# Optimization experiments

Measured on AMD Instinct MI355X. Metric: run time of the kernel, lower is better.

Reference implementation:

```python
import jax, jax.numpy as jnp
import numpy as np

B, S, D, H, E, F = 2, 1024, 1024, 16, 8, 4096
HD = D // H
EPS = 1e-5


def setup_inputs() -> dict:
    key = jax.random.key(0)
    ks = jax.random.split(key, 16)
    sc = 0.02
    return {
        "src": jax.random.normal(ks[0], (B, S, D), jnp.float32),
        "in_proj_w": jax.random.normal(ks[1], (3 * D, D), jnp.float32) * sc,
        "in_proj_b": jnp.zeros((3 * D,), jnp.float32),
        "out_w": jax.random.normal(ks[2], (D, D), jnp.float32) * sc,
        "out_b": jnp.zeros((D,), jnp.float32),
        "gate_w": jax.random.normal(ks[3], (E, D), jnp.float32) * sc,
        "gate_b": jnp.zeros((E,), jnp.float32),
        "w1": jax.random.normal(ks[4], (E, F, D), jnp.float32) * sc,
        "b1": jnp.zeros((E, F), jnp.float32),
        "w2": jax.random.normal(ks[5], (E, D, F), jnp.float32) * sc,
        "b2": jnp.zeros((E, D), jnp.float32),
        "ln1_g": jnp.ones((D,), jnp.float32),
        "ln1_b": jnp.zeros((D,), jnp.float32),
        "ln2_g": jnp.ones((D,), jnp.float32),
        "ln2_b": jnp.zeros((D,), jnp.float32),
    }


def layer_norm(x, g, b):
    mu = jnp.mean(x, axis=-1, keepdims=True)
    var = jnp.mean(jnp.square(x - mu), axis=-1, keepdims=True)
    return (x - mu) * jax.lax.rsqrt(var + EPS) * g + b


def mha(x, in_proj_w, in_proj_b, out_w, out_b):
    # torch nn.MultiheadAttention, batch_first, self-attention, eval mode
    qkv = x @ in_proj_w.T + in_proj_b  # (B,S,3D)
    q, k, v = jnp.split(qkv, 3, axis=-1)
    q = q.reshape(B, S, H, HD).transpose(0, 2, 1, 3)  # bhsd
    k = k.reshape(B, S, H, HD).transpose(0, 2, 1, 3)
    v = v.reshape(B, S, H, HD).transpose(0, 2, 1, 3)
    scores = jnp.einsum("bhqd,bhkd->bhqk", q, k) / np.sqrt(HD).astype(np.float32)
    attn = jax.nn.softmax(scores, axis=-1)
    o = jnp.einsum("bhqk,bhkd->bhqd", attn, v)
    o = o.transpose(0, 2, 1, 3).reshape(B, S, D)
    return o @ out_w.T + out_b


def moe(x, gate_w, gate_b, w1, b1, w2, b2, top_k=2):
    gate_logits = x @ gate_w.T + gate_b  # (B,S,E)
    topk_logits, topk_idx = jax.lax.top_k(gate_logits, top_k)
    topk_probs = jax.nn.softmax(topk_logits, axis=-1)  # (B,S,K)
    # dense per-expert weight: prob if in top-k else 0
    onehot = jax.nn.one_hot(topk_idx, E, dtype=x.dtype)  # (B,S,K,E)
    w_dense = jnp.einsum("bske,bsk->bse", onehot, topk_probs)
    # faithful to original: all experts computed densely, then mask-weighted
    h = jnp.einsum("bsd,efd->besf", x, w1) + b1[None, :, None, :]
    h = jax.nn.gelu(h, approximate=False)
    eo = jnp.einsum("besf,edf->besd", h, w2) + b2[None, :, None, :]
    out = jnp.einsum("besd,bse->bsd", eo, w_dense)
    usage = jnp.mean(jax.nn.softmax(gate_logits, axis=-1), axis=(0, 1))
    aux_loss = E * jnp.sum(usage ** 2)
    return out, aux_loss


def reference(src, in_proj_w, in_proj_b, out_w, out_b, gate_w, gate_b,
              w1, b1, w2, b2, ln1_g, ln1_b, ln2_g, ln2_b):
    attn_out = mha(src, in_proj_w, in_proj_b, out_w, out_b)
    x = layer_norm(src + attn_out, ln1_g, ln1_b)
    moe_out, aux_loss = moe(x, gate_w, gate_b, w1, b1, w2, b2)
    x = layer_norm(x + moe_out, ln2_g, ln2_b)
    return x, aux_loss
```

## Files before the change

### kernel.cpp

```cpp
#include <hip/hip_runtime.h>
#include <stdint.h>
#include <stddef.h>

#define T_TOK 2048
#define DMODEL 1024
#define NHEAD 16
#define HDIM 64
#define NEXP 8
#define FDIM 4096
#define SLEN 1024
#define NBATCH 2
#define LN_EPS 1e-5f

typedef unsigned short u16;
typedef __attribute__((ext_vector_type(8))) short s16x8;
typedef __attribute__((ext_vector_type(4))) float f32x4;
typedef __attribute__((ext_vector_type(4))) unsigned short u16x4;
typedef __attribute__((ext_vector_type(8))) unsigned short u16x8;

typedef __attribute__((address_space(1))) void gvoid;
typedef __attribute__((address_space(3))) void lvoid;

__device__ __forceinline__ u16 f2bf(float x) {
  union { float f; unsigned int u; } v; v.f = x;
  unsigned int r = v.u + 0x7fffu + ((v.u >> 16) & 1u);
  return (u16)(r >> 16);
}

__device__ __forceinline__ void gl_lds16(const u16* g, u16* lds_base) {
  __builtin_amdgcn_global_load_lds((gvoid*)g, (lvoid*)lds_base, 16, 0, 0);
}

__device__ __forceinline__ void cvt_body(const float* __restrict__ x,
                                         u16* __restrict__ y, long n4) {
  long i = (long)blockIdx.x * 256 + threadIdx.x;
  if (i >= n4) return;
  float4 v = ((const float4*)x)[i];
  u16x4 o;
  o[0] = f2bf(v.x); o[1] = f2bf(v.y); o[2] = f2bf(v.z); o[3] = f2bf(v.w);
  ((u16x4*)y)[i] = o;
}
__global__ __launch_bounds__(256) void cvt_small(const float* x, u16* y, long n4) { cvt_body(x, y, n4); }
__global__ __launch_bounds__(256) void cvt_w1(const float* x, u16* y, long n4) { cvt_body(x, y, n4); }
__global__ __launch_bounds__(256) void cvt_w2(const float* x, u16* y, long n4) { cvt_body(x, y, n4); }

template<int BM, int OUTBF, int DOGELU>
__device__ __forceinline__ void gemm_body(
    const u16* __restrict__ A, long lda,
    const u16* __restrict__ Bp, long ldb,
    char* __restrict__ C, long ldc,
    const float* __restrict__ bias,
    int Mloc, int k0start, int Kc, int m0, int n0) {
  constexpr int AS_BYTES = 2 * BM * 64 * 2;
  constexpr int SMEM_BYTES = AS_BYTES + 2 * 128 * 64 * 2;
  __shared__ __align__(16) char smem[SMEM_BYTES];
  u16 (*As)[BM][64]  = reinterpret_cast<u16(*)[BM][64]>(smem);
  u16 (*Bs)[128][64] = reinterpret_cast<u16(*)[128][64]>(smem + AS_BYTES);

  constexpr int SM = BM / 32;
  constexpr int LPI = BM / 32 + 4;

  int tid = threadIdx.x;
  int lane = tid & 63, w = tid >> 6;
  int lrow = lane >> 3;
  int sg8 = ((lane & 7) ^ lrow) * 8;
  int q = lane >> 4, rr = lane & 15;
  int wm = (w & 1) * (BM / 2), wn = (w >> 1) * 64;
  int NIT = Kc >> 6;

  auto issue = [&](int kt, int b) {
    int k0 = k0start + (kt << 6);
    for (int p = 0; p < BM / 32; p++) {
      int rb = p * 32 + w * 8;
      int gr = m0 + rb + lrow; if (gr > Mloc - 1) gr = Mloc - 1;
      gl_lds16(A + (long)gr * lda + k0 + sg8, &As[b][rb][0]);
    }
    for (int p = 0; p < 4; p++) {
      int rb = p * 32 + w * 8;
      gl_lds16(Bp + (long)(n0 + rb + lrow) * ldb + k0 + sg8, &Bs[b][rb][0]);
    }
  };

  f32x4 acc[SM][4];
  for (int i = 0; i < SM; i++)
    for (int j = 0; j < 4; j++)
      for (int r = 0; r < 4; r++) acc[i][j][r] = 0.f;

  issue(0, 0);
  if (NIT > 1) issue(1, 1);

  int slot0 = ((q ^ (rr & 7)) * 8);
  int slot1 = (((4 + q) ^ (rr & 7)) * 8);

  for (int kt = 0; kt < NIT; kt++) {
    int b = kt & 1;
    if (kt + 1 < NIT)
      asm volatile("s_waitcnt vmcnt(%0)" :: "i"(LPI) : "memory");
    else
      asm volatile("s_waitcnt vmcnt(0)" ::: "memory");
    asm volatile("s_barrier" ::: "memory");

    s16x8 a0[SM], a1[SM], b0[4], b1[4];
    for (int i = 0; i < SM; i++) {
      a0[i] = *(const s16x8*)&As[b][wm + i * 16 + rr][slot0];
      a1[i] = *(const s16x8*)&As[b][wm + i * 16 + rr][slot1];
    }
    for (int j = 0; j < 4; j++) {
      b0[j] = *(const s16x8*)&Bs[b][wn + j * 16 + rr][slot0];
      b1[j] = *(const s16x8*)&Bs[b][wn + j * 16 + rr][slot1];
    }
    asm volatile("s_waitcnt lgkmcnt(0)" ::: "memory");
    asm volatile("s_barrier" ::: "memory");
    if (kt + 2 < NIT) issue(kt + 2, b);

    for (int i = 0; i < SM; i++)
      for (int j = 0; j < 4; j++) {
        acc[i][j] = __builtin_amdgcn_mfma_f32_16x16x32_bf16(a0[i], b0[j], acc[i][j], 0, 0, 0);
        acc[i][j] = __builtin_amdgcn_mfma_f32_16x16x32_bf16(a1[i], b1[j], acc[i][j], 0, 0, 0);
      }
  }

  u16*   Cu = (u16*)smem;
  float* Cf = (float*)smem;
  for (int i = 0; i < SM; i++)
    for (int j = 0; j < 4; j++) {
      int col = wn + j * 16 + rr;
      float bv = bias ? bias[n0 + col] : 0.f;
      for (int r = 0; r < 4; r++) {
        int row = wm + i * 16 + q * 4 + r;
        float v = acc[i][j][r] + bv;
        if (DOGELU) v = 0.5f * v * (1.f + erff(v * 0.70710678118f));
        if (OUTBF) Cu[row * 128 + col] = f2bf(v);
        else       Cf[row * 128 + col] = v;
      }
    }
  __syncthreads();
  if (OUTBF) {
    for (int p = 0; p < BM / 16; p++) {
      int row = p * 16 + (tid >> 4);
      int co  = (tid & 15) * 8;
      if (m0 + row < Mloc) {
        u16x8 vv = *(const u16x8*)&Cu[row * 128 + co];
        *(u16x8*)((u16*)C + (long)(m0 + row) * ldc + n0 + co) = vv;
      }
    }
  } else {
    for (int p = 0; p < BM / 8; p++) {
      int row = p * 8 + (tid >> 5);
      int co  = (tid & 31) * 4;
      if (m0 + row < Mloc) {
        float4 vv = *(const float4*)&Cf[row * 128 + co];
        *(float4*)((float*)C + (long)(m0 + row) * ldc + n0 + co) = vv;
      }
    }
  }
}

__global__ __launch_bounds__(256) void k_qkv(const u16* __restrict__ A,
                                             const u16* __restrict__ B,
                                             u16* __restrict__ C,
                                             const float* __restrict__ bias) {
  gemm_body<64, 1, 0>(A, DMODEL, B, DMODEL, (char*)C, 3 * DMODEL, bias,
                      T_TOK, 0, DMODEL, blockIdx.y * 64, blockIdx.x * 128);
}

__global__ __launch_bounds__(256) void k_outp(const u16* __restrict__ A,
                                              const u16* __restrict__ B,
                                              float* __restrict__ Cpart) {
  int z = blockIdx.z;
  char* C = (char*)(Cpart + (long)z * T_TOK * DMODEL);
  gemm_body<64, 0, 0>(A, DMODEL, B, DMODEL, C, DMODEL, nullptr,
                      T_TOK, z * 512, 512, blockIdx.y * 64, blockIdx.x * 128);
}

__global__ __launch_bounds__(256) void k_ffn1(const u16* __restrict__ Ag,
                                              const u16* __restrict__ Bg,
                                              u16* __restrict__ Cg,
                                              const float* __restrict__ biasg,
                                              const int* __restrict__ cntp,
                                              const int* __restrict__ offp) {
  int z = blockIdx.z;
  int Mloc = cntp[z];
  int m0 = blockIdx.y * 128;
  if (m0 >= Mloc) return;
  long o = offp[z];
  gemm_body<128, 1, 1>(Ag + o * DMODEL, DMODEL,
                       Bg + (long)z * FDIM * DMODEL, DMODEL,
                       (char*)(Cg + o * FDIM), FDIM,
                       biasg + (long)z * FDIM,
                       Mloc, 0, DMODEL, m0, blockIdx.x * 128);
}

__global__ __launch_bounds__(256) void k_ffn2(const u16* __restrict__ Ag,
                                              const u16* __restrict__ Bg,
                                              float* __restrict__ Cg,
                                              const float* __restrict__ biasg,
                                              const int* __restrict__ cntp,
                                              const int* __restrict__ offp) {
  int z = blockIdx.z;
  int Mloc = cntp[z];
  int m0 = blockIdx.y * 64;
  if (m0 >= Mloc) return;
  long o = offp[z];
  gemm_body<64, 0, 0>(Ag + o * FDIM, FDIM,
                      Bg + (long)z * DMODEL * FDIM, FDIM,
                      (char*)(Cg + o * DMODEL), DMODEL,
                      biasg + (long)z * DMODEL,
                      Mloc, 0, FDIM, m0, blockIdx.x * 128);
}

__global__ __launch_bounds__(256) void transpose_v(const u16* __restrict__ qkv,
                                                   u16* __restrict__ vt) {
  __shared__ u16 tile[64][65];
  int s0 = blockIdx.x * 64, bh = blockIdx.y;
  int b = bh >> 4, h = bh & 15;
  int r = threadIdx.x >> 3, c = (threadIdx.x & 7) * 8;
  for (int p = 0; p < 64; p += 32) {
    u16x8 v = *(const u16x8*)&qkv[(long)(b * SLEN + s0 + p + r) * 3072 + 2048 + h * 64 + c];
    for (int j = 0; j < 8; j++) tile[p + r][c + j] = v[j];
  }
  __syncthreads();
  for (int p = 0; p < 64; p += 32) {
    int d = p + r;
    u16x8 v;
    for (int j = 0; j < 8; j++) v[j] = tile[c + j][d];
    *(u16x8*)&vt[((long)bh * 64 + d) * SLEN + s0 + c] = v;
  }
}

__global__ __launch_bounds__(256) void fused_attn(const u16* __restrict__ qkv,
                                                  const u16* __restrict__ vt,
                                                  u16* __restrict__ o2) {
  __shared__ u16 Qs[128][64];
  __shared__ u16 Ks[64][64];
  __shared__ u16 Vs[64][64];
  __shared__ u16 Ps[128][72];

  int qt = blockIdx.x, bh = blockIdx.y;
  int b = bh >> 4, h = bh & 15;
  const u16* base = qkv + (long)b * SLEN * 3072 + h * 64;
  const u16* vbase = vt + (long)bh * HDIM * SLEN;

  int tid = threadIdx.x, lane = tid & 63, w = tid >> 6;
  int lrow = lane >> 3;
  int sg8 = ((lane & 7) ^ lrow) * 8;
  int q = lane >> 4, rr = lane & 15;
  int wm = w * 32;

  for (int p = 0; p < 4; p++) {
    int rb = p * 32 + w * 8;
    gl_lds16(base + (long)(qt * 128 + rb + lrow) * 3072 + sg8, &Qs[rb][0]);
  }

  f32x4 O[2][4];
  float mi[2][4], li[2][4];
  for (int i = 0; i < 2; i++)
    for (int r = 0; r < 4; r++) { mi[i][r] = -1e30f; li[i][r] = 0.f; }
  for (int i = 0; i < 2; i++)
    for (int jn = 0; jn < 4; jn++)
      for (int r = 0; r < 4; r++) O[i][jn][r] = 0.f;

  for (int kt = 0; kt < 16; kt++) {
    __syncthreads();
    for (int p = 0; p < 2; p++) {
      int rb = p * 32 + w * 8;
      gl_lds16(base + (long)(kt * 64 + rb + lrow) * 3072 + 1024 + sg8, &Ks[rb][0]);
      gl_lds16(vbase + (long)(rb + lrow) * SLEN + kt * 64 + sg8, &Vs[rb][0]);
    }
    __syncthreads();

    f32x4 S[2][4];
    for (int i = 0; i < 2; i++)
      for (int j = 0; j < 4; j++)
        for (int r = 0; r < 4; r++) S[i][j][r] = 0.f;
    for (int ks = 0; ks < 2; ks++) {
      int slot = (((ks * 4 + q) ^ (rr & 7)) * 8);
      s16x8 aq0 = *(const s16x8*)&Qs[wm + rr][slot];
      s16x8 aq1 = *(const s16x8*)&Qs[wm + 16 + rr][slot];
      for (int j = 0; j < 4; j++) {
        s16x8 bk = *(const s16x8*)&Ks[j * 16 + rr][slot];
        S[0][j] = __builtin_amdgcn_mfma_f32_16x16x32_bf16(aq0, bk, S[0][j], 0, 0, 0);
        S[1][j] = __builtin_amdgcn_mfma_f32_16x16x32_bf16(aq1, bk, S[1][j], 0, 0, 0);
      }
    }

    for (int i = 0; i < 2; i++) {
      for (int r = 0; r < 4; r++) {
        float mx = -1e30f;
        for (int j = 0; j < 4; j++) mx = fmaxf(mx, S[i][j][r]);
        for (int o = 1; o < 16; o <<= 1) mx = fmaxf(mx, __shfl_xor(mx, o));
        mx *= 0.125f;
        float mnew = fmaxf(mi[i][r], mx);
        float al = __expf(mi[i][r] - mnew);
        mi[i][r] = mnew;
        float ps = 0.f;
        for (int j = 0; j < 4; j++) {
          float e = __expf(S[i][j][r] * 0.125f - mnew);
          S[i][j][r] = e;
          ps += e;
        }
        for (int o = 1; o < 16; o <<= 1) ps += __shfl_xor(ps, o);
        li[i][r] = li[i][r] * al + ps;
        for (int jn = 0; jn < 4; jn++) O[i][jn][r] *= al;
      }
    }

    for (int i = 0; i < 2; i++)
      for (int j = 0; j < 4; j++)
        for (int r = 0; r < 4; r++)
          Ps[wm + i * 16 + q * 4 + r][j * 16 + rr] = f2bf(S[i][j][r]);
    __syncthreads();

    for (int ks = 0; ks < 2; ks++) {
      s16x8 ap0 = *(const s16x8*)&Ps[wm + rr][ks * 32 + q * 8];
      s16x8 ap1 = *(const s16x8*)&Ps[wm + 16 + rr][ks * 32 + q * 8];
      int slot = (((ks * 4 + q) ^ (rr & 7)) * 8);
      for (int jn = 0; jn < 4; jn++) {
        s16x8 bv = *(const s16x8*)&Vs[jn * 16 + rr][slot];
        O[0][jn] = __builtin_amdgcn_mfma_f32_16x16x32_bf16(ap0, bv, O[0][jn], 0, 0, 0);
        O[1][jn] = __builtin_amdgcn_mfma_f32_16x16x32_bf16(ap1, bv, O[1][jn], 0, 0, 0);
      }
    }
  }

  __syncthreads();
  u16* Pf = &Ps[0][0];
  for (int i = 0; i < 2; i++)
    for (int r = 0; r < 4; r++) {
      float inv = 1.f / li[i][r];
      int row = wm + i * 16 + q * 4 + r;
      for (int jn = 0; jn < 4; jn++)
        Pf[row * 64 + jn * 16 + rr] = f2bf(O[i][jn][r] * inv);
    }
  __syncthreads();
  for (int p = 0; p < 4; p++) {
    int row = p * 32 + (tid >> 3);
    int co  = (tid & 7) * 8;
    u16x8 vv = *(const u16x8*)&Pf[row * 64 + co];
    int s = qt * 128 + row;
    *(u16x8*)&o2[((long)(b * SLEN + s)) * DMODEL + h * 64 + co] = vv;
  }
}

__global__ __launch_bounds__(256) void add_ln(const float* __restrict__ a,
                                              const float* __restrict__ p0,
                                              const float* __restrict__ p1,
                                              const float* __restrict__ ob,
                                              const float* __restrict__ g,
                                              const float* __restrict__ bb,
                                              float* __restrict__ xf, u16* __restrict__ xb) {
  int t = blockIdx.x, tid = threadIdx.x;
  float4 va = ((const float4*)(a + (long)t * DMODEL))[tid];
  float4 v0v = ((const float4*)(p0 + (long)t * DMODEL))[tid];
  float4 v1v = ((const float4*)(p1 + (long)t * DMODEL))[tid];
  float4 vo = ((const float4*)ob)[tid];
  float v0 = va.x + v0v.x + v1v.x + vo.x;
  float v1 = va.y + v0v.y + v1v.y + vo.y;
  float v2 = va.z + v0v.z + v1v.z + vo.z;
  float v3 = va.w + v0v.w + v1v.w + vo.w;
  float s = v0 + v1 + v2 + v3;
  float s2 = v0 * v0 + v1 * v1 + v2 * v2 + v3 * v3;
  __shared__ float sa[4], sb[4];
  for (int o = 32; o; o >>= 1) { s += __shfl_down(s, o); s2 += __shfl_down(s2, o); }
  int lane = tid & 63, w = tid >> 6;
  if (lane == 0) { sa[w] = s; sb[w] = s2; }
  __syncthreads();
  s = sa[0] + sa[1] + sa[2] + sa[3];
  s2 = sb[0] + sb[1] + sb[2] + sb[3];
  float mu = s * (1.f / DMODEL);
  float var = s2 * (1.f / DMODEL) - mu * mu;
  float rs = rsqrtf(var + LN_EPS);
  float4 gg = ((const float4*)g)[tid];
  float4 bv = ((const float4*)bb)[tid];
  float4 o;
  o.x = (v0 - mu) * rs * gg.x + bv.x;
  o.y = (v1 - mu) * rs * gg.y + bv.y;
  o.z = (v2 - mu) * rs * gg.z + bv.z;
  o.w = (v3 - mu) * rs * gg.w + bv.w;
  ((float4*)(xf + (long)t * DMODEL))[tid] = o;
  u16x4 obv;
  obv[0] = f2bf(o.x); obv[1] = f2bf(o.y); obv[2] = f2bf(o.z); obv[3] = f2bf(o.w);
  ((u16x4*)(xb + (long)t * DMODEL))[tid] = obv;
}

__global__ __launch_bounds__(256) void gate_kernel(
    const float* __restrict__ xf, const float* __restrict__ gw, const float* __restrict__ gb,
    int* __restrict__ cnt, int* __restrict__ tok_list,
    int* __restrict__ tk_e, int* __restrict__ tk_pos, float* __restrict__ tk_prob,
    float* __restrict__ usage) {
  int wid = threadIdx.x >> 6, lane = threadIdx.x & 63;
  int t = blockIdx.x * 4 + wid;
  float xv[16];
  for (int j = 0; j < 16; j++) xv[j] = xf[(long)t * DMODEL + j * 64 + lane];
  float l[8];
  for (int e = 0; e < 8; e++) {
    float d = 0.f;
    for (int j = 0; j < 16; j++) d += xv[j] * gw[e * DMODEL + j * 64 + lane];
    for (int o = 32; o; o >>= 1) d += __shfl_down(d, o);
    l[e] = d;
  }
  __shared__ float us[8];
  if (threadIdx.x < 8) us[threadIdx.x] = 0.f;
  __syncthreads();
  if (lane == 0) {
    float mx = -1e30f;
    for (int e = 0; e < 8; e++) { l[e] += gb[e]; mx = fmaxf(mx, l[e]); }
    float ex[8], sum = 0.f;
    for (int e = 0; e < 8; e++) { ex[e] = expf(l[e] - mx); sum += ex[e]; }
    float inv = 1.f / sum;
    for (int e = 0; e < 8; e++) atomicAdd(&us[e], ex[e] * inv);
    int i1 = 0;
    for (int e = 1; e < 8; e++) if (l[e] > l[i1]) i1 = e;
    int i2 = (i1 == 0) ? 1 : 0;
    for (int e = 0; e < 8; e++) if (e != i1 && l[e] > l[i2]) i2 = e;
    float bb = expf(l[i2] - l[i1]);
    float p1 = 1.f / (1.f + bb), p2 = bb / (1.f + bb);
    int pos1 = atomicAdd(&cnt[i1], 1);
    tok_list[i1 * 2048 + pos1] = t;
    tk_e[2 * t] = i1; tk_pos[2 * t] = pos1; tk_prob[2 * t] = p1;
    int pos2 = atomicAdd(&cnt[i2], 1);
    tok_list[i2 * 2048 + pos2] = t;
    tk_e[2 * t + 1] = i2; tk_pos[2 * t + 1] = pos2; tk_prob[2 * t + 1] = p2;
  }
  __syncthreads();
  if (threadIdx.x < 8) atomicAdd(&usage[threadIdx.x], us[threadIdx.x]);
}

__global__ void finalize_gate(const int* __restrict__ cnt, int* __restrict__ offp,
                              const float* __restrict__ usage, float* __restrict__ aux_out) {
  if (threadIdx.x == 0) {
    int o = 0;
    for (int e = 0; e < 8; e++) { offp[e] = o; o += cnt[e]; }
    float s = 0.f;
    for (int e = 0; e < 8; e++) { float u = usage[e] * (1.f / T_TOK); s += u * u; }
    aux_out[0] = (float)NEXP * s;
  }
}

__global__ __launch_bounds__(256) void gather_x(const u16* __restrict__ xb,
                                                const int* __restrict__ cnt,
                                                const int* __restrict__ offp,
                                                const int* __restrict__ tok_list,
                                                u16* __restrict__ xg) {
  int e = blockIdx.y, i = blockIdx.x;
  if (i >= cnt[e]) return;
  int t = tok_list[e * 2048 + i];
  long j = offp[e] + i;
  ((uint2*)(xg + j * DMODEL))[threadIdx.x] =
      ((const uint2*)(xb + (long)t * DMODEL))[threadIdx.x];
}

__global__ __launch_bounds__(256) void moe_ln2(
    const float* __restrict__ xf, const float* __restrict__ y,
    const int* __restrict__ offp, const int* __restrict__ tk_e,
    const int* __restrict__ tk_pos, const float* __restrict__ tk_prob,
    const float* __restrict__ g, const float* __restrict__ bb, float* __restrict__ out) {
  int t = blockIdx.x, tid = threadIdx.x;
  int e0 = tk_e[2 * t], e1 = tk_e[2 * t + 1];
  long j0 = (long)offp[e0] + tk_pos[2 * t];
  long j1 = (long)offp[e1] + tk_pos[2 * t + 1];
  float p0 = tk_prob[2 * t], p1 = tk_prob[2 * t + 1];
  float4 vx = ((const float4*)(xf + (long)t * DMODEL))[tid];
  float4 y0 = ((const float4*)(y + j0 * DMODEL))[tid];
  float4 y1 = ((const float4*)(y + j1 * DMODEL))[tid];
  float v0 = vx.x + p0 * y0.x + p1 * y1.x;
  float v1 = vx.y + p0 * y0.y + p1 * y1.y;
  float v2 = vx.z + p0 * y0.z + p1 * y1.z;
  float v3 = vx.w + p0 * y0.w + p1 * y1.w;
  float s = v0 + v1 + v2 + v3;
  float s2 = v0 * v0 + v1 * v1 + v2 * v2 + v3 * v3;
  __shared__ float sa[4], sb[4];
  for (int o = 32; o; o >>= 1) { s += __shfl_down(s, o); s2 += __shfl_down(s2, o); }
  int lane = tid & 63, w = tid >> 6;
  if (lane == 0) { sa[w] = s; sb[w] = s2; }
  __syncthreads();
  s = sa[0] + sa[1] + sa[2] + sa[3];
  s2 = sb[0] + sb[1] + sb[2] + sb[3];
  float mu = s * (1.f / DMODEL);
  float var = s2 * (1.f / DMODEL) - mu * mu;
  float rs = rsqrtf(var + LN_EPS);
  float4 gg = ((const float4*)g)[tid];
  float4 bv = ((const float4*)bb)[tid];
  float4 o;
  o.x = (v0 - mu) * rs * gg.x + bv.x;
  o.y = (v1 - mu) * rs * gg.y + bv.y;
  o.z = (v2 - mu) * rs * gg.z + bv.z;
  o.w = (v3 - mu) * rs * gg.w + bv.w;
  ((float4*)(out + (long)t * DMODEL))[tid] = o;
}

extern "C" void kernel_launch(void* const* d_in, const int* in_sizes, int n_in,
                              void* d_out, int out_size, void* d_ws, size_t ws_size,
                              hipStream_t stream) {
  const float* src  = (const float*)d_in[0];
  const float* inw  = (const float*)d_in[1];
  const float* inb  = (const float*)d_in[2];
  const float* outw = (const float*)d_in[3];
  const float* outb = (const float*)d_in[4];
  const float* gw   = (const float*)d_in[5];
  const float* gb   = (const float*)d_in[6];
  const float* w1   = (const float*)d_in[7];
  const float* b1   = (const float*)d_in[8];
  const float* w2   = (const float*)d_in[9];
  const float* b2   = (const float*)d_in[10];
  const float* g1   = (const float*)d_in[11];
  const float* bb1  = (const float*)d_in[12];
  const float* g2   = (const float*)d_in[13];
  const float* bb2  = (const float*)d_in[14];
  float* out = (float*)d_out;

  char* w = (char*)d_ws;
  auto alloc = [&](size_t bytes) {
    char* p = w;
    w += (bytes + 255) & ~(size_t)255;
    return p;
  };

  int*   cnt     = (int*)alloc(8 * 4);
  int*   offp    = (int*)alloc(8 * 4);
  float* usage   = (float*)alloc(8 * 4);
  int*   tok_list= (int*)alloc((size_t)NEXP * 2048 * 4);
  int*   tk_e    = (int*)alloc((size_t)2 * T_TOK * 4);
  int*   tk_pos  = (int*)alloc((size_t)2 * T_TOK * 4);
  float* tk_prob = (float*)alloc((size_t)2 * T_TOK * 4);

  u16* src_bf  = (u16*)alloc((size_t)T_TOK * DMODEL * 2);
  u16* inw_bf  = (u16*)alloc((size_t)3 * DMODEL * DMODEL * 2);
  u16* outw_bf = (u16*)alloc((size_t)DMODEL * DMODEL * 2);
  u16* w1_bf   = (u16*)alloc((size_t)NEXP * FDIM * DMODEL * 2);
  u16* w2_bf   = (u16*)alloc((size_t)NEXP * DMODEL * FDIM * 2);
  u16* qkv_bf  = (u16*)alloc((size_t)T_TOK * 3 * DMODEL * 2);
  u16* vt_bf   = (u16*)alloc((size_t)T_TOK * DMODEL * 2);
  u16* o2_bf   = (u16*)alloc((size_t)T_TOK * DMODEL * 2);
  float* attn_p= (float*)alloc((size_t)2 * T_TOK * DMODEL * 4);
  float* x_f   = (float*)alloc((size_t)T_TOK * DMODEL * 4);
  u16* x_bf    = (u16*)alloc((size_t)T_TOK * DMODEL * 2);
  u16* xg_bf   = (u16*)alloc((size_t)2 * T_TOK * DMODEL * 2);
  u16* h_bf    = (u16*)alloc((size_t)2 * T_TOK * FDIM * 2);
  float* y_f   = (float*)alloc((size_t)2 * T_TOK * DMODEL * 4);
  (void)ws_size; (void)n_in; (void)in_sizes; (void)out_size;

  hipMemsetAsync(cnt, 0, 3 * 256, stream);

  cvt_small<<<(T_TOK * DMODEL / 4 + 255) / 256, 256, 0, stream>>>(src, src_bf, T_TOK * DMODEL / 4);
  cvt_small<<<(3 * DMODEL * DMODEL / 4 + 255) / 256, 256, 0, stream>>>(inw, inw_bf, 3L * DMODEL * DMODEL / 4);
  cvt_small<<<(DMODEL * DMODEL / 4 + 255) / 256, 256, 0, stream>>>(outw, outw_bf, (long)DMODEL * DMODEL / 4);
  cvt_w1<<<(int)((long)NEXP * FDIM * DMODEL / 4 / 256), 256, 0, stream>>>(w1, w1_bf, (long)NEXP * FDIM * DMODEL / 4);
  cvt_w2<<<(int)((long)NEXP * DMODEL * FDIM / 4 / 256), 256, 0, stream>>>(w2, w2_bf, (long)NEXP * DMODEL * FDIM / 4);

  k_qkv<<<dim3(24, 32), 256, 0, stream>>>(src_bf, inw_bf, qkv_bf, inb);

  transpose_v<<<dim3(16, 32), 256, 0, stream>>>(qkv_bf, vt_bf);

  fused_attn<<<dim3(8, 32), 256, 0, stream>>>(qkv_bf, vt_bf, o2_bf);

  k_outp<<<dim3(8, 32, 2), 256, 0, stream>>>(o2_bf, outw_bf, attn_p);

  add_ln<<<T_TOK, 256, 0, stream>>>(src, attn_p, attn_p + (long)T_TOK * DMODEL,
                                    outb, g1, bb1, x_f, x_bf);

  gate_kernel<<<T_TOK / 4, 256, 0, stream>>>(x_f, gw, gb, cnt, tok_list,
                                             tk_e, tk_pos, tk_prob, usage);
  finalize_gate<<<1, 64, 0, stream>>>(cnt, offp, usage, out + (long)T_TOK * DMODEL);

  gather_x<<<dim3(2048, 8), 256, 0, stream>>>(x_bf, cnt, offp, tok_list, xg_bf);

  k_ffn1<<<dim3(32, 16, 8), 256, 0, stream>>>(xg_bf, w1_bf, h_bf, b1, cnt, offp);

  k_ffn2<<<dim3(8, 32, 8), 256, 0, stream>>>(h_bf, w2_bf, y_f, b2, cnt, offp);

  moe_ln2<<<T_TOK, 256, 0, stream>>>(x_f, y_f, offp, tk_e, tk_pos, tk_prob,
                                     g2, bb2, out);
}
```

Measured before the change: 672.0 us.

## Split-K FFN2 with larger tiles and double-buffer K/V loads in attention

FFN2 is split into two K halves, each written to a separate fp32 partial buffer using 128-row tiles. The partials and the expert bias are summed inside the final LayerNorm kernel. Attention now double-buffers K/V tiles in LDS, prefetching the next tile during compute, and drops one barrier per iteration. This adds extra fp32 partial-buffer traffic and LDS use in exchange for better tile reuse and load/compute overlap.

```diff
diff --git a/kernel.cpp b/kernel.cpp
--- a/kernel.cpp
+++ b/kernel.cpp
@@ -193,20 +193,21 @@
 
 __global__ __launch_bounds__(256) void k_ffn2(const u16* __restrict__ Ag,
                                               const u16* __restrict__ Bg,
-                                              float* __restrict__ Cg,
-                                              const float* __restrict__ biasg,
+                                              float* __restrict__ Cpart,
                                               const int* __restrict__ cntp,
                                               const int* __restrict__ offp) {
-  int z = blockIdx.z;
+  int zz = blockIdx.z;
+  int z = zz & 7, kh = zz >> 3;
   int Mloc = cntp[z];
-  int m0 = blockIdx.y * 64;
+  int m0 = blockIdx.y * 128;
   if (m0 >= Mloc) return;
   long o = offp[z];
-  gemm_body<64, 0, 0>(Ag + o * FDIM, FDIM,
-                      Bg + (long)z * DMODEL * FDIM, FDIM,
-                      (char*)(Cg + o * DMODEL), DMODEL,
-                      biasg + (long)z * DMODEL,
-                      Mloc, 0, FDIM, m0, blockIdx.x * 128);
+  float* C = Cpart + (long)kh * 2 * T_TOK * DMODEL;
+  gemm_body<128, 0, 0>(Ag + o * FDIM, FDIM,
+                       Bg + (long)z * DMODEL * FDIM, FDIM,
+                       (char*)(C + o * DMODEL), DMODEL,
+                       nullptr,
+                       Mloc, kh * 2048, 2048, m0, blockIdx.x * 128);
 }
 
 __global__ __launch_bounds__(256) void transpose_v(const u16* __restrict__ qkv,
@@ -232,8 +233,8 @@
                                                   const u16* __restrict__ vt,
                                                   u16* __restrict__ o2) {
   __shared__ u16 Qs[128][64];
-  __shared__ u16 Ks[64][64];
-  __shared__ u16 Vs[64][64];
+  __shared__ u16 Ks[2][64][64];
+  __shared__ u16 Vs[2][64][64];
   __shared__ u16 Ps[128][72];
 
   int qt = blockIdx.x, bh = blockIdx.y;
@@ -247,10 +248,19 @@
   int q = lane >> 4, rr = lane & 15;
   int wm = w * 32;
 
+  auto issue_kv = [&](int kt, int bf) {
+    for (int p = 0; p < 2; p++) {
+      int rb = p * 32 + w * 8;
+      gl_lds16(base + (long)(kt * 64 + rb + lrow) * 3072 + 1024 + sg8, &Ks[bf][rb][0]);
+      gl_lds16(vbase + (long)(rb + lrow) * SLEN + kt * 64 + sg8, &Vs[bf][rb][0]);
+    }
+  };
+
   for (int p = 0; p < 4; p++) {
     int rb = p * 32 + w * 8;
     gl_lds16(base + (long)(qt * 128 + rb + lrow) * 3072 + sg8, &Qs[rb][0]);
   }
+  issue_kv(0, 0);
 
   f32x4 O[2][4];
   float mi[2][4], li[2][4];
@@ -261,13 +271,10 @@
       for (int r = 0; r < 4; r++) O[i][jn][r] = 0.f;
 
   for (int kt = 0; kt < 16; kt++) {
-    __syncthreads();
-    for (int p = 0; p < 2; p++) {
-      int rb = p * 32 + w * 8;
-      gl_lds16(base + (long)(kt * 64 + rb + lrow) * 3072 + 1024 + sg8, &Ks[rb][0]);
-      gl_lds16(vbase + (long)(rb + lrow) * SLEN + kt * 64 + sg8, &Vs[rb][0]);
-    }
-    __syncthreads();
+    int bf = kt & 1;
+    asm volatile("s_waitcnt vmcnt(0)" ::: "memory");
+    asm volatile("s_barrier" ::: "memory");
+    if (kt + 1 < 16) issue_kv(kt + 1, bf ^ 1);
 
     f32x4 S[2][4];
     for (int i = 0; i < 2; i++)
@@ -278,7 +285,7 @@
       s16x8 aq0 = *(const s16x8*)&Qs[wm + rr][slot];
       s16x8 aq1 = *(const s16x8*)&Qs[wm + 16 + rr][slot];
       for (int j = 0; j < 4; j++) {
-        s16x8 bk = *(const s16x8*)&Ks[j * 16 + rr][slot];
+        s16x8 bk = *(const s16x8*)&Ks[bf][j * 16 + rr][slot];
         S[0][j] = __builtin_amdgcn_mfma_f32_16x16x32_bf16(aq0, bk, S[0][j], 0, 0, 0);
         S[1][j] = __builtin_amdgcn_mfma_f32_16x16x32_bf16(aq1, bk, S[1][j], 0, 0, 0);
       }
@@ -309,14 +316,13 @@
       for (int j = 0; j < 4; j++)
         for (int r = 0; r < 4; r++)
           Ps[wm + i * 16 + q * 4 + r][j * 16 + rr] = f2bf(S[i][j][r]);
-    __syncthreads();
 
     for (int ks = 0; ks < 2; ks++) {
       s16x8 ap0 = *(const s16x8*)&Ps[wm + rr][ks * 32 + q * 8];
       s16x8 ap1 = *(const s16x8*)&Ps[wm + 16 + rr][ks * 32 + q * 8];
       int slot = (((ks * 4 + q) ^ (rr & 7)) * 8);
       for (int jn = 0; jn < 4; jn++) {
-        s16x8 bv = *(const s16x8*)&Vs[jn * 16 + rr][slot];
+        s16x8 bv = *(const s16x8*)&Vs[bf][jn * 16 + rr][slot];
         O[0][jn] = __builtin_amdgcn_mfma_f32_16x16x32_bf16(ap0, bv, O[0][jn], 0, 0, 0);
         O[1][jn] = __builtin_amdgcn_mfma_f32_16x16x32_bf16(ap1, bv, O[1][jn], 0, 0, 0);
       }
@@ -452,21 +458,27 @@
 
 __global__ __launch_bounds__(256) void moe_ln2(
     const float* __restrict__ xf, const float* __restrict__ y,
+    const float* __restrict__ b2g,
     const int* __restrict__ offp, const int* __restrict__ tk_e,
     const int* __restrict__ tk_pos, const float* __restrict__ tk_prob,
     const float* __restrict__ g, const float* __restrict__ bb, float* __restrict__ out) {
+  const long HALF = (long)2 * T_TOK * DMODEL;
   int t = blockIdx.x, tid = threadIdx.x;
   int e0 = tk_e[2 * t], e1 = tk_e[2 * t + 1];
   long j0 = (long)offp[e0] + tk_pos[2 * t];
   long j1 = (long)offp[e1] + tk_pos[2 * t + 1];
   float p0 = tk_prob[2 * t], p1 = tk_prob[2 * t + 1];
   float4 vx = ((const float4*)(xf + (long)t * DMODEL))[tid];
-  float4 y0 = ((const float4*)(y + j0 * DMODEL))[tid];
-  float4 y1 = ((const float4*)(y + j1 * DMODEL))[tid];
-  float v0 = vx.x + p0 * y0.x + p1 * y1.x;
-  float v1 = vx.y + p0 * y0.y + p1 * y1.y;
-  float v2 = vx.z + p0 * y0.z + p1 * y1.z;
-  float v3 = vx.w + p0 * y0.w + p1 * y1.w;
+  float4 y0a = ((const float4*)(y + j0 * DMODEL))[tid];
+  float4 y0b = ((const float4*)(y + HALF + j0 * DMODEL))[tid];
+  float4 y1a = ((const float4*)(y + j1 * DMODEL))[tid];
+  float4 y1b = ((const float4*)(y + HALF + j1 * DMODEL))[tid];
+  float4 b0v = ((const float4*)(b2g + (long)e0 * DMODEL))[tid];
+  float4 b1v = ((const float4*)(b2g + (long)e1 * DMODEL))[tid];
+  float v0 = vx.x + p0 * (y0a.x + y0b.x + b0v.x) + p1 * (y1a.x + y1b.x + b1v.x);
+  float v1 = vx.y + p0 * (y0a.y + y0b.y + b0v.y) + p1 * (y1a.y + y1b.y + b1v.y);
+  float v2 = vx.z + p0 * (y0a.z + y0b.z + b0v.z) + p1 * (y1a.z + y1b.z + b1v.z);
+  float v3 = vx.w + p0 * (y0a.w + y0b.w + b0v.w) + p1 * (y1a.w + y1b.w + b1v.w);
   float s = v0 + v1 + v2 + v3;
   float s2 = v0 * v0 + v1 * v1 + v2 * v2 + v3 * v3;
   __shared__ float sa[4], sb[4];
@@ -537,7 +549,7 @@
   u16* x_bf    = (u16*)alloc((size_t)T_TOK * DMODEL * 2);
   u16* xg_bf   = (u16*)alloc((size_t)2 * T_TOK * DMODEL * 2);
   u16* h_bf    = (u16*)alloc((size_t)2 * T_TOK * FDIM * 2);
-  float* y_f   = (float*)alloc((size_t)2 * T_TOK * DMODEL * 4);
+  float* y_f   = (float*)alloc((size_t)4 * T_TOK * DMODEL * 4);
   (void)ws_size; (void)n_in; (void)in_sizes; (void)out_size;
 
   hipMemsetAsync(cnt, 0, 3 * 256, stream);
@@ -567,8 +579,8 @@
 
   k_ffn1<<<dim3(32, 16, 8), 256, 0, stream>>>(xg_bf, w1_bf, h_bf, b1, cnt, offp);
 
-  k_ffn2<<<dim3(8, 32, 8), 256, 0, stream>>>(h_bf, w2_bf, y_f, b2, cnt, offp);
-
-  moe_ln2<<<T_TOK, 256, 0, stream>>>(x_f, y_f, offp, tk_e, tk_pos, tk_prob,
+  k_ffn2<<<dim3(8, 16, 16), 256, 0, stream>>>(h_bf, w2_bf, y_f, cnt, offp);
+
+  moe_ln2<<<T_TOK, 256, 0, stream>>>(x_f, y_f, b2, offp, tk_e, tk_pos, tk_prob,
                                      g2, bb2, out);
 }
```

After: 645.8 us. 3.9% less time.
